# Kernel tuning notes

Hardware: AMD Instinct MI355X
Metric: run time of the kernel (lower is better)

The kernel has to match this reference:

```python
import jax, jax.numpy as jnp
import numpy as np

N = 100000      # nodes_num
E = 1600000     # edges (avg degree 16)
D_IN = 256
D_OUT = 128
EPS = 1e-3      # keras BatchNormalization default epsilon
LEAKY = 0.2     # tf.nn.leaky_relu default alpha


def setup_inputs() -> dict:
    key = jax.random.key(0)
    ks = jax.random.split(key, 6)
    x = jax.random.normal(ks[0], (N, D_IN), jnp.float32)
    w = jax.random.normal(ks[1], (D_IN, D_OUT), jnp.float32) / np.float32(np.sqrt(D_IN))
    w1 = jax.random.normal(ks[2], (D_IN, D_IN), jnp.float32) / np.float32(np.sqrt(D_IN))
    w2 = jax.random.normal(ks[3], (D_IN, D_IN), jnp.float32) / np.float32(np.sqrt(D_IN))
    rows = jnp.sort(jax.random.randint(ks[4], (E,), 0, N, jnp.int32))
    cols = jax.random.randint(ks[5], (E,), 0, N, jnp.int32)
    edge_vals = jnp.ones((E,), jnp.float32)
    return {"x": x, "w": w, "w1": w1, "w2": w2,
            "edge_vals": edge_vals, "rows": rows, "cols": cols}


def reference(x, w, w1, w2, edge_vals, rows, cols):
    # Batch norm (training mode: per-feature stats over node axis, gamma=1, beta=0)
    mean = jnp.mean(x, axis=0)
    var = jnp.var(x, axis=0)
    xn = (x - mean) * jax.lax.rsqrt(var + EPS)          # [N, D_IN]

    mapped = xn @ w                                      # [N, D_OUT]
    s1 = jnp.tanh(jnp.sum((xn @ w1) * xn, axis=1))       # [N] row score
    s2 = jnp.tanh(jnp.sum((xn @ w2) * xn, axis=1))       # [N] col score

    # sparse add of adj*s1[row] and adj*s2[col], then leaky_relu on edge values
    ev = edge_vals * (s1[rows] + s2[cols])               # [E]
    ev = jnp.where(ev > 0, ev, LEAKY * ev)

    # tf.sparse.softmax: softmax over the nonzero entries of each row
    m = jax.ops.segment_max(ev, rows, num_segments=N)    # [N]
    m = jnp.where(jnp.isfinite(m), m, 0.0)               # empty rows -> 0
    ex = jnp.exp(ev - m[rows])
    denom = jax.ops.segment_sum(ex, rows, num_segments=N)
    alpha = ex / denom[rows]                             # [E] edge softmax

    # SpMM: out[i] = sum_{e: rows[e]==i} alpha[e] * mapped[cols[e]]
    out = jax.ops.segment_sum(alpha[:, None] * mapped[cols], rows, num_segments=N)
    return out  # activation is identity (activation=None)
```

## Files before the change

kernel.cpp:

```cpp
#include <hip/hip_runtime.h>

#define D_IN 256
#define D_OUT 128
#define EPS_BN 1e-3f
#define LEAKY 0.2f

typedef unsigned short u16;
typedef unsigned int u32;
typedef u16 u16x4 __attribute__((ext_vector_type(4)));
typedef u16 u16x8 __attribute__((ext_vector_type(8)));
typedef __bf16 bf16x8 __attribute__((ext_vector_type(8)));
typedef float f32x4 __attribute__((ext_vector_type(4)));

__device__ __forceinline__ float bf2f(u16 u) {
    u32 v = ((u32)u) << 16;
    return __uint_as_float(v);
}
__device__ __forceinline__ u16 f2bf(float f) {
    u32 u = __float_as_uint(f);
    u32 r = (u + 0x7FFFu + ((u >> 16) & 1u)) >> 16;
    return (u16)r;
}

__device__ __forceinline__ void bar_lgkm() {
    asm volatile("s_waitcnt lgkmcnt(0)" ::: "memory");
    __builtin_amdgcn_s_barrier();
    asm volatile("" ::: "memory");
}

__global__ void colstats_k(const float* __restrict__ x, int n,
                           float* __restrict__ sums, float* __restrict__ sqs) {
    int c = threadIdx.x;
    float s = 0.f, q = 0.f;
    for (int r = blockIdx.x; r < n; r += gridDim.x) {
        float v = x[(size_t)r * D_IN + c];
        s += v;
        q += v * v;
    }
    atomicAdd(&sums[c], s);
    atomicAdd(&sqs[c], q);
}

__global__ void finalize_k(const float* __restrict__ sums, const float* __restrict__ sqs,
                           int n, float* __restrict__ mean, float* __restrict__ inv) {
    int c = threadIdx.x;
    float m = sums[c] / (float)n;
    float v = sqs[c] / (float)n - m * m;
    mean[c] = m;
    inv[c] = rsqrtf(v + EPS_BN);
}

__global__ void prep_w_k(const float* __restrict__ w1, const float* __restrict__ w2,
                         const float* __restrict__ w, u16* __restrict__ Bth,
                         u16* __restrict__ Btl, u16* __restrict__ Wth,
                         u16* __restrict__ Wtl) {
    int idx = blockIdx.x * 256 + threadIdx.x;
    int k = idx & 255;
    int nn = idx >> 8;
    if (nn < 512) {
        float v = (nn < 256) ? w1[(size_t)k * 256 + nn]
                             : w2[(size_t)k * 256 + (nn - 256)];
        u16 h = f2bf(v);
        u16 l = f2bf(v - bf2f(h));
        Bth[(size_t)nn * 256 + k] = h;
        Btl[(size_t)nn * 256 + k] = l;
    } else {
        int nm = nn - 512;
        float v = w[(size_t)k * D_OUT + nm];
        u16 h = f2bf(v);
        u16 l = f2bf(v - bf2f(h));
        Wth[(size_t)nm * 256 + k] = h;
        Wtl[(size_t)nm * 256 + k] = l;
    }
}

__device__ __forceinline__ int kmap(int v, int g, int j) {
    return (v == 0) ? (8 * g + j) : (16 * (j >> 2) + 4 * g + (j & 3));
}

__global__ void probe_k(int* __restrict__ flagp) {
    __shared__ float Ar[16][32];
    __shared__ float Br[32][16];
    __shared__ float Dr[16][16];
    int l = threadIdx.x;
    for (int i = l; i < 512; i += 64) {
        int r = i >> 5, k = i & 31;
        Ar[r][k] = (float)(((r * 5 + k * 3) % 11) - 5);
    }
    for (int i = l; i < 512; i += 64) {
        int k = i >> 4, c = i & 15;
        Br[k][c] = (float)(((k * 3 + c * 7) % 13) - 6);
    }
    __syncthreads();
    for (int i = l; i < 256; i += 64) {
        int r = i >> 4, c = i & 15;
        float s = 0.f;
        for (int k = 0; k < 32; ++k) s += Ar[r][k] * Br[k][c];
        Dr[r][c] = s;
    }
    __syncthreads();
    int g = l >> 4, c15 = l & 15;
    int found = -1;
    for (int combo = 0; combo < 4; ++combo) {
        int va = combo >> 1, vb = combo & 1;
        u16x8 af, bfv;
#pragma unroll
        for (int j = 0; j < 8; ++j) {
            af[j] = f2bf(Ar[c15][kmap(va, g, j)]);
            bfv[j] = f2bf(Br[kmap(vb, g, j)][c15]);
        }
        f32x4 d = {0.f, 0.f, 0.f, 0.f};
        d = __builtin_amdgcn_mfma_f32_16x16x32_bf16(
            __builtin_bit_cast(bf16x8, af), __builtin_bit_cast(bf16x8, bfv), d,
            0, 0, 0);
        bool ok = true;
#pragma unroll
        for (int r = 0; r < 4; ++r) ok = ok && (d[r] == Dr[g * 4 + r][c15]);
        if (found < 0 && __all(ok)) found = combo;
    }
    if (l == 0) flagp[0] = (found < 0) ? 0 : found;
}

__device__ __forceinline__ void stage_A(const float* __restrict__ x,
                                        const float* __restrict__ mean,
                                        const float* __restrict__ inv, int m0,
                                        int n, u16* Ah, u16* Al) {
    const int tid = threadIdx.x;
    for (int i = 0; i < 16; ++i) {
        int chunk = tid + (i << 8);
        int r = chunk >> 6;
        int c4 = (chunk & 63) << 2;
        int gr = m0 + r;
        bool ok = gr < n;
        float4 v = make_float4(0.f, 0.f, 0.f, 0.f);
        if (ok) v = *(const float4*)(x + (size_t)gr * D_IN + c4);
        float4 mn = *(const float4*)(mean + c4);
        float4 iv = *(const float4*)(inv + c4);
        float a0 = ok ? (v.x - mn.x) * iv.x : 0.f;
        float a1 = ok ? (v.y - mn.y) * iv.y : 0.f;
        float a2 = ok ? (v.z - mn.z) * iv.z : 0.f;
        float a3 = ok ? (v.w - mn.w) * iv.w : 0.f;
        u16 h0 = f2bf(a0), h1 = f2bf(a1), h2 = f2bf(a2), h3 = f2bf(a3);
        u16 l0 = f2bf(a0 - bf2f(h0)), l1 = f2bf(a1 - bf2f(h1));
        u16 l2 = f2bf(a2 - bf2f(h2)), l3 = f2bf(a3 - bf2f(h3));
        int off = (r << 9) + (((c4 << 1) ^ ((r & 7) << 4)));
        u16x4 hv = {h0, h1, h2, h3};
        u16x4 lv = {l0, l1, l2, l3};
        *(u16x4*)((char*)Ah + off) = hv;
        *(u16x4*)((char*)Al + off) = lv;
    }
}

__device__ __forceinline__ void ldb_regs(const u16* __restrict__ Gh,
                                         const u16* __restrict__ Gl, int n0,
                                         int k0, int tid, u16x8 (&hv)[2],
                                         u16x8 (&lv)[2]) {
#pragma unroll
    for (int i = 0; i < 2; ++i) {
        int chunk = tid + (i << 8);
        int nl = chunk >> 3;
        int k8 = (chunk & 7) << 3;
        size_t goff = (size_t)(n0 + nl) * 256 + k0 + k8;
        hv[i] = *(const u16x8*)(Gh + goff);
        lv[i] = *(const u16x8*)(Gl + goff);
    }
}
__device__ __forceinline__ void stb_lds(u16* Bh, u16* Bl, int tid,
                                        const u16x8 (&hv)[2],
                                        const u16x8 (&lv)[2]) {
#pragma unroll
    for (int i = 0; i < 2; ++i) {
        int chunk = tid + (i << 8);
        int nl = chunk >> 3;
        int k8 = (chunk & 7) << 3;
        int off = (nl << 7) + (((k8 << 1) ^ ((nl & 7) << 4)));
        *(u16x8*)((char*)Bh + off) = hv[i];
        *(u16x8*)((char*)Bl + off) = lv[i];
    }
}

template <int V>
__device__ __forceinline__ bf16x8 ld_frag(const u16* plane, int rowByteBase,
                                          int swz, int kbyte, int g) {
    const char* p = (const char*)plane + rowByteBase;
    if constexpr (V == 0) {
        u16x8 v = *(const u16x8*)(p + ((kbyte + (g << 4)) ^ swz));
        return __builtin_bit_cast(bf16x8, v);
    } else {
        u16x4 a = *(const u16x4*)(p + ((kbyte + (g << 3)) ^ swz));
        u16x4 b = *(const u16x4*)(p + ((kbyte + 32 + (g << 3)) ^ swz));
        u16x8 v;
        v[0] = a[0]; v[1] = a[1]; v[2] = a[2]; v[3] = a[3];
        v[4] = b[0]; v[5] = b[1]; v[6] = b[2]; v[7] = b[3];
        return __builtin_bit_cast(bf16x8, v);
    }
}

template <int VA, int VB>
__device__ __forceinline__ void comp_kt(const u16* Ah, const u16* Al,
                                        const u16* Bh, const u16* Bl, int kt,
                                        int wm, int wn, int c15, int g,
                                        f32x4 (&acc)[2][2]) {
#pragma unroll
    for (int kk = 0; kk < 2; ++kk) {
        int kbA = kt * 128 + kk * 64;
        int kbB = kk * 64;
        bf16x8 ah[2], alf[2], bhf[2], blf[2];
#pragma unroll
        for (int mf = 0; mf < 2; ++mf) {
            int row = wm * 32 + mf * 16 + c15;
            int swz = (row & 7) << 4;
            ah[mf] = ld_frag<VA>(Ah, row << 9, swz, kbA, g);
            alf[mf] = ld_frag<VA>(Al, row << 9, swz, kbA, g);
        }
#pragma unroll
        for (int nf = 0; nf < 2; ++nf) {
            int nl = wn * 32 + nf * 16 + c15;
            int swz = (nl & 7) << 4;
            bhf[nf] = ld_frag<VB>(Bh, nl << 7, swz, kbB, g);
            blf[nf] = ld_frag<VB>(Bl, nl << 7, swz, kbB, g);
        }
#pragma unroll
        for (int mf = 0; mf < 2; ++mf)
#pragma unroll
            for (int nf = 0; nf < 2; ++nf) {
                acc[mf][nf] = __builtin_amdgcn_mfma_f32_16x16x32_bf16(
                    ah[mf], bhf[nf], acc[mf][nf], 0, 0, 0);
                acc[mf][nf] = __builtin_amdgcn_mfma_f32_16x16x32_bf16(
                    ah[mf], blf[nf], acc[mf][nf], 0, 0, 0);
                acc[mf][nf] = __builtin_amdgcn_mfma_f32_16x16x32_bf16(
                    alf[mf], bhf[nf], acc[mf][nf], 0, 0, 0);
            }
    }
}

template <int VA, int VB>
__device__ __forceinline__ void quadmap_body(
    const float* __restrict__ x, const u16* __restrict__ Bth,
    const u16* __restrict__ Btl, const u16* __restrict__ Wth,
    const u16* __restrict__ Wtl, const float* __restrict__ mean,
    const float* __restrict__ inv, float* __restrict__ s1,
    float* __restrict__ s2, u16* __restrict__ mapped, int n, int mapCT,
    u16* Ah, u16* Al, u16* Bh, u16* Bl) {
    const int tid = threadIdx.x;
    const int lane = tid & 63, wave = tid >> 6;
    const int g = lane >> 4, c15 = lane & 15;
    const int wm = wave >> 1, wn = wave & 1;
    const int m0 = blockIdx.x * 64;

    stage_A(x, mean, inv, m0, n, Ah, Al);
    __syncthreads();

    u16x8 rbh[2], rbl[2];
    ldb_regs(Bth, Btl, 0, 0, tid, rbh, rbl);

    float sp[2][4] = {{0.f, 0.f, 0.f, 0.f}, {0.f, 0.f, 0.f, 0.f}};

    for (int jt = 0; jt < 8; ++jt) {
        f32x4 acc[2][2];
#pragma unroll
        for (int mf = 0; mf < 2; ++mf)
#pragma unroll
            for (int nf = 0; nf < 2; ++nf) acc[mf][nf] = (f32x4){0.f, 0.f, 0.f, 0.f};

        for (int kt = 0; kt < 4; ++kt) {
            bar_lgkm();
            stb_lds(Bh, Bl, tid, rbh, rbl);
            const u16 *sH, *sL;
            int nn0, nk0;
            if (kt < 3)      { sH = Bth; sL = Btl; nn0 = jt * 64;       nk0 = (kt + 1) * 64; }
            else if (jt < 7) { sH = Bth; sL = Btl; nn0 = (jt + 1) * 64; nk0 = 0; }
            else             { sH = Wth; sL = Wtl; nn0 = 0;             nk0 = 0; }
            ldb_regs(sH, sL, nn0, nk0, tid, rbh, rbl);
            bar_lgkm();
            comp_kt<VA, VB>(Ah, Al, Bh, Bl, kt, wm, wn, c15, g, acc);
        }

        int fcol0 = (jt & 3) << 6;
#pragma unroll
        for (int mf = 0; mf < 2; ++mf) {
#pragma unroll
            for (int nf = 0; nf < 2; ++nf) {
                int col = fcol0 + wn * 32 + nf * 16 + c15;
                float mn = mean[col], ivv = inv[col];
#pragma unroll
                for (int r = 0; r < 4; ++r) {
                    int grow = m0 + wm * 32 + mf * 16 + g * 4 + r;
                    float xv = 0.f;
                    if (grow < n) xv = (x[(size_t)grow * D_IN + col] - mn) * ivv;
                    sp[mf][r] = fmaf(acc[mf][nf][r], xv, sp[mf][r]);
                }
            }
        }
        if ((jt & 3) == 3) {
            float part[2][4];
#pragma unroll
            for (int mf = 0; mf < 2; ++mf)
#pragma unroll
                for (int r = 0; r < 4; ++r) {
                    float v = sp[mf][r];
                    v += __shfl_xor(v, 1);
                    v += __shfl_xor(v, 2);
                    v += __shfl_xor(v, 4);
                    v += __shfl_xor(v, 8);
                    part[mf][r] = v;
                    sp[mf][r] = 0.f;
                }
            float* scratch = (float*)Bh;
            bar_lgkm();
            if (c15 == 0) {
#pragma unroll
                for (int mf = 0; mf < 2; ++mf)
#pragma unroll
                    for (int r = 0; r < 4; ++r) {
                        int sidx = (((((wm << 2) | g) << 1) | mf) << 3) | (r << 1) | wn;
                        scratch[sidx] = part[mf][r];
                    }
            }
            bar_lgkm();
            if (wn == 0 && c15 == 0) {
                float* dst = (jt < 4) ? s1 : s2;
#pragma unroll
                for (int mf = 0; mf < 2; ++mf)
#pragma unroll
                    for (int r = 0; r < 4; ++r) {
                        int sidx = (((((wm << 2) | g) << 1) | mf) << 3) | (r << 1);
                        float tot = scratch[sidx] + scratch[sidx | 1];
                        int grow = m0 + wm * 32 + mf * 16 + g * 4 + r;
                        if (grow < n) dst[grow] = tanhf(tot);
                    }
            }
        }
    }

    const int tiles = mapCT >> 6;
    for (int t = 0; t < tiles; ++t) {
        f32x4 acc[2][2];
#pragma unroll
        for (int mf = 0; mf < 2; ++mf)
#pragma unroll
            for (int nf = 0; nf < 2; ++nf) acc[mf][nf] = (f32x4){0.f, 0.f, 0.f, 0.f};

        for (int kt = 0; kt < 4; ++kt) {
            bar_lgkm();
            stb_lds(Bh, Bl, tid, rbh, rbl);
            int nn0 = (kt < 3) ? t * 64 : ((t + 1 < tiles) ? (t + 1) * 64 : t * 64);
            int nk0 = (kt < 3) ? (kt + 1) * 64 : 0;
            ldb_regs(Wth, Wtl, nn0, nk0, tid, rbh, rbl);
            bar_lgkm();
            comp_kt<VA, VB>(Ah, Al, Bh, Bl, kt, wm, wn, c15, g, acc);
        }
#pragma unroll
        for (int mf = 0; mf < 2; ++mf)
#pragma unroll
            for (int nf = 0; nf < 2; ++nf) {
                int si = t * 64 + wn * 32 + nf * 16 + c15;
#pragma unroll
                for (int r = 0; r < 4; ++r) {
                    int grow = m0 + wm * 32 + mf * 16 + g * 4 + r;
                    if (grow < n)
                        mapped[(size_t)grow * mapCT + si] = f2bf(acc[mf][nf][r]);
                }
            }
    }
}

__global__ __launch_bounds__(256) void quadmap_mfma_k(
    const float* __restrict__ x, const u16* __restrict__ Bth,
    const u16* __restrict__ Btl, const u16* __restrict__ Wth,
    const u16* __restrict__ Wtl, const float* __restrict__ mean,
    const float* __restrict__ inv, float* __restrict__ s1,
    float* __restrict__ s2, u16* __restrict__ mapped,
    const int* __restrict__ flagp, int n, int mapCT) {
    __shared__ u16 Ah[64 * 256];
    __shared__ u16 Al[64 * 256];
    __shared__ u16 Bh[64 * 64];
    __shared__ u16 Bl[64 * 64];
    int v = flagp[0];
    if (v == 1)
        quadmap_body<0, 1>(x, Bth, Btl, Wth, Wtl, mean, inv, s1, s2, mapped, n, mapCT, Ah, Al, Bh, Bl);
    else if (v == 2)
        quadmap_body<1, 0>(x, Bth, Btl, Wth, Wtl, mean, inv, s1, s2, mapped, n, mapCT, Ah, Al, Bh, Bl);
    else if (v == 3)
        quadmap_body<1, 1>(x, Bth, Btl, Wth, Wtl, mean, inv, s1, s2, mapped, n, mapCT, Ah, Al, Bh, Bl);
    else
        quadmap_body<0, 0>(x, Bth, Btl, Wth, Wtl, mean, inv, s1, s2, mapped, n, mapCT, Ah, Al, Bh, Bl);
}

template <int VA, int VB>
__device__ __forceinline__ void map_body(
    const float* __restrict__ x, const u16* __restrict__ Wth,
    const u16* __restrict__ Wtl, const float* __restrict__ mean,
    const float* __restrict__ inv, u16* __restrict__ mapped, int n, int c0,
    int CT, u16* Ah, u16* Al, u16* Bh, u16* Bl) {
    const int tid = threadIdx.x;
    const int lane = tid & 63, wave = tid >> 6;
    const int g = lane >> 4, c15 = lane & 15;
    const int wm = wave >> 1, wn = wave & 1;
    const int m0 = blockIdx.x * 64;

    stage_A(x, mean, inv, m0, n, Ah, Al);
    __syncthreads();

    u16x8 rbh[2], rbl[2];
    ldb_regs(Wth, Wtl, c0, 0, tid, rbh, rbl);

    const int tiles = CT >> 6;
    for (int t = 0; t < tiles; ++t) {
        f32x4 acc[2][2];
#pragma unroll
        for (int mf = 0; mf < 2; ++mf)
#pragma unroll
            for (int nf = 0; nf < 2; ++nf) acc[mf][nf] = (f32x4){0.f, 0.f, 0.f, 0.f};

        for (int kt = 0; kt < 4; ++kt) {
            bar_lgkm();
            stb_lds(Bh, Bl, tid, rbh, rbl);
            int nn0 = (kt < 3) ? c0 + t * 64
                               : c0 + ((t + 1 < tiles) ? (t + 1) * 64 : t * 64);
            int nk0 = (kt < 3) ? (kt + 1) * 64 : 0;
            ldb_regs(Wth, Wtl, nn0, nk0, tid, rbh, rbl);
            bar_lgkm();
            comp_kt<VA, VB>(Ah, Al, Bh, Bl, kt, wm, wn, c15, g, acc);
        }
#pragma unroll
        for (int mf = 0; mf < 2; ++mf)
#pragma unroll
            for (int nf = 0; nf < 2; ++nf) {
                int si = t * 64 + wn * 32 + nf * 16 + c15;
#pragma unroll
                for (int r = 0; r < 4; ++r) {
                    int grow = m0 + wm * 32 + mf * 16 + g * 4 + r;
                    if (grow < n) mapped[(size_t)grow * CT + si] = f2bf(acc[mf][nf][r]);
                }
            }
    }
}

__global__ __launch_bounds__(256) void map_mfma_k(
    const float* __restrict__ x, const u16* __restrict__ Wth,
    const u16* __restrict__ Wtl, const float* __restrict__ mean,
    const float* __restrict__ inv, u16* __restrict__ mapped, int n, int c0,
    int CT, const int* __restrict__ flagp) {
    __shared__ u16 Ah[64 * 256];
    __shared__ u16 Al[64 * 256];
    __shared__ u16 Bh[64 * 64];
    __shared__ u16 Bl[64 * 64];
    int v = flagp[0];
    if (v == 1) map_body<0, 1>(x, Wth, Wtl, mean, inv, mapped, n, c0, CT, Ah, Al, Bh, Bl);
    else if (v == 2) map_body<1, 0>(x, Wth, Wtl, mean, inv, mapped, n, c0, CT, Ah, Al, Bh, Bl);
    else if (v == 3) map_body<1, 1>(x, Wth, Wtl, mean, inv, mapped, n, c0, CT, Ah, Al, Bh, Bl);
    else map_body<0, 0>(x, Wth, Wtl, mean, inv, mapped, n, c0, CT, Ah, Al, Bh, Bl);
}

template <typename OT>
__global__ __launch_bounds__(256) void gemm_map_k(const float* __restrict__ x,
                                                  const float* __restrict__ w,
                                                  const float* __restrict__ mean,
                                                  const float* __restrict__ inv,
                                                  OT* __restrict__ outp, int n,
                                                  int c0, int CT) {
    __shared__ float As[64][68];
    __shared__ float Bs[64][68];
    const int tid = threadIdx.x;
    const int tx = tid & 15, ty = tid >> 4;
    const int m0 = blockIdx.x * 64;
    const int tiles = (CT + 63) >> 6;

    for (int t = 0; t < tiles; ++t) {
        const int jt = c0 + (t << 6);
        float acc[4][4];
#pragma unroll
        for (int a = 0; a < 4; ++a)
#pragma unroll
            for (int b = 0; b < 4; ++b) acc[a][b] = 0.f;

        for (int kt = 0; kt < D_IN; kt += 64) {
#pragma unroll
            for (int i = 0; i < 4; ++i) {
                int f4 = tid + 256 * i;
                int r = f4 >> 4;
                int c4 = (f4 & 15) << 2;
                float4 o;
                int gr = m0 + r;
                if (gr < n) {
                    float4 v = *(const float4*)(x + (size_t)gr * D_IN + kt + c4);
                    float4 mn = *(const float4*)(mean + kt + c4);
                    float4 iv = *(const float4*)(inv + kt + c4);
                    o.x = (v.x - mn.x) * iv.x;
                    o.y = (v.y - mn.y) * iv.y;
                    o.z = (v.z - mn.z) * iv.z;
                    o.w = (v.w - mn.w) * iv.w;
                } else {
                    o = make_float4(0.f, 0.f, 0.f, 0.f);
                }
                *(float4*)&As[r][c4] = o;
            }
#pragma unroll
            for (int i = 0; i < 4; ++i) {
                int f4 = tid + 256 * i;
                int r = f4 >> 4;
                int c4 = (f4 & 15) << 2;
                int jc = jt + c4;
                float4 bv = (jc < D_OUT)
                                ? *(const float4*)(w + (size_t)(kt + r) * D_OUT + jc)
                                : make_float4(0.f, 0.f, 0.f, 0.f);
                *(float4*)&Bs[r][c4] = bv;
            }
            __syncthreads();
#pragma unroll 8
            for (int k = 0; k < 64; ++k) {
                float4 bv = *(const float4*)&Bs[k][tx << 2];
                float a0 = As[(ty << 2) + 0][k];
                float a1 = As[(ty << 2) + 1][k];
                float a2 = As[(ty << 2) + 2][k];
                float a3 = As[(ty << 2) + 3][k];
                acc[0][0] = fmaf(a0, bv.x, acc[0][0]);
                acc[0][1] = fmaf(a0, bv.y, acc[0][1]);
                acc[0][2] = fmaf(a0, bv.z, acc[0][2]);
                acc[0][3] = fmaf(a0, bv.w, acc[0][3]);
                acc[1][0] = fmaf(a1, bv.x, acc[1][0]);
                acc[1][1] = fmaf(a1, bv.y, acc[1][1]);
                acc[1][2] = fmaf(a1, bv.z, acc[1][2]);
                acc[1][3] = fmaf(a1, bv.w, acc[1][3]);
                acc[2][0] = fmaf(a2, bv.x, acc[2][0]);
                acc[2][1] = fmaf(a2, bv.y, acc[2][1]);
                acc[2][2] = fmaf(a2, bv.z, acc[2][2]);
                acc[2][3] = fmaf(a2, bv.w, acc[2][3]);
                acc[3][0] = fmaf(a3, bv.x, acc[3][0]);
                acc[3][1] = fmaf(a3, bv.y, acc[3][1]);
                acc[3][2] = fmaf(a3, bv.z, acc[3][2]);
                acc[3][3] = fmaf(a3, bv.w, acc[3][3]);
            }
            __syncthreads();
        }
        int si = (jt - c0) + (tx << 2);
        if (si < CT) {
#pragma unroll
            for (int a = 0; a < 4; ++a) {
                int gm = m0 + (ty << 2) + a;
                if (gm < n) {
                    ushort4 pk;
                    pk.x = f2bf(acc[a][0]);
                    pk.y = f2bf(acc[a][1]);
                    pk.z = f2bf(acc[a][2]);
                    pk.w = f2bf(acc[a][3]);
                    *(ushort4*)((u16*)outp + (size_t)gm * CT + si) = pk;
                }
            }
        }
    }
}

__global__ void build_rowptr_k(const int* __restrict__ rows, int E, int n,
                               int* __restrict__ rp) {
    int e = blockIdx.x * blockDim.x + threadIdx.x;
    if (e >= E) return;
    int r = rows[e];
    int prev = (e == 0) ? -1 : rows[e - 1];
    for (int q = prev + 1; q <= r; ++q) rp[q] = e;
    if (e == E - 1) {
        for (int q = r + 1; q <= n; ++q) rp[q] = E;
    }
}

template <bool WRITE_ALPHA>
__global__ __launch_bounds__(256) void row_softmax_k(
    const int* __restrict__ row_ptr, const int* __restrict__ cols,
    const float* __restrict__ ev, const float* __restrict__ s1,
    const float* __restrict__ s2, float* __restrict__ rmax,
    float* __restrict__ rsm, float* __restrict__ alpha, int n) {
    int wave = threadIdx.x >> 6;
    int lane = threadIdx.x & 63;
    int row = blockIdx.x * 4 + wave;
    if (row >= n) return;
    int e0 = row_ptr[row], e1 = row_ptr[row + 1];
    if (e0 >= e1) {
        if (lane == 0) {
            rmax[row] = 0.f;
            rsm[row] = 0.f;
        }
        return;
    }
    float s1r = s1[row];
    float mx = -1e30f;
    for (int e = e0 + lane; e < e1; e += 64) {
        float v = ev[e] * (s1r + s2[cols[e]]);
        v = v > 0.f ? v : LEAKY * v;
        mx = fmaxf(mx, v);
    }
#pragma unroll
    for (int off = 32; off; off >>= 1) mx = fmaxf(mx, __shfl_xor(mx, off));
    float sm = 0.f;
    for (int e = e0 + lane; e < e1; e += 64) {
        float v = ev[e] * (s1r + s2[cols[e]]);
        v = v > 0.f ? v : LEAKY * v;
        sm += __expf(v - mx);
    }
#pragma unroll
    for (int off = 32; off; off >>= 1) sm += __shfl_xor(sm, off);
    float rsm_v = 1.f / sm;
    if (lane == 0) {
        rmax[row] = mx;
        rsm[row] = rsm_v;
    }
    if constexpr (WRITE_ALPHA) {
        for (int e = e0 + lane; e < e1; e += 64) {
            float v = ev[e] * (s1r + s2[cols[e]]);
            v = v > 0.f ? v : LEAKY * v;
            alpha[e] = __expf(v - mx) * rsm_v;
        }
    }
}

template <bool HAS_ALPHA>
__global__ __launch_bounds__(256) void attn_gather2_k(
    const int* __restrict__ row_ptr, const int* __restrict__ cols,
    const float* __restrict__ alpha, const float* __restrict__ ev,
    const float* __restrict__ s1, const float* __restrict__ s2,
    const float* __restrict__ rmax, const float* __restrict__ rsm,
    const u16* __restrict__ mapped, float* __restrict__ outp, int n, int c0,
    int CT) {
    const int wave = threadIdx.x >> 6;
    const int lane = threadIdx.x & 63;
    const int row = blockIdx.x * 4 + wave;
    if (row >= n) return;
    const int e0 = row_ptr[row], e1 = row_ptr[row + 1];
    float* orow = outp + (size_t)row * D_OUT + c0;
    const int nu = CT >> 1;
    const bool act = lane < nu;
    if (e0 >= e1) {
        if (act) *(float2*)(orow + (lane << 1)) = make_float2(0.f, 0.f);
        return;
    }
    float s1r = 0.f, mxv = 0.f, rsv = 0.f;
    if constexpr (!HAS_ALPHA) {
        s1r = s1[row];
        mxv = rmax[row];
        rsv = rsm[row];
    }
    const u32* map32 = (const u32*)mapped;
    float ox = 0.f, oy = 0.f;
    int e = e0;
    while (e < e1) {
        int cnt = min(e1 - e, 64);
        int ce = 0;
        float ae = 0.f;
        if (lane < cnt) {
            int ee = e + lane;
            ce = cols[ee];
            if constexpr (HAS_ALPHA) {
                ae = alpha[ee];
            } else {
                float v = ev[ee] * (s1r + s2[ce]);
                v = v > 0.f ? v : LEAKY * v;
                ae = __expf(v - mxv) * rsv;
            }
        }
        for (int j0 = 0; j0 < cnt; j0 += 8) {
            int cv[8];
            float av[8];
            u32 mv[8];
#pragma unroll
            for (int j = 0; j < 8; ++j) {
                cv[j] = __shfl(ce, j0 + j);
                av[j] = __shfl(ae, j0 + j);
            }
#pragma unroll
            for (int j = 0; j < 8; ++j)
                mv[j] = act ? map32[(size_t)cv[j] * nu + lane] : 0u;
#pragma unroll
            for (int j = 0; j < 8; ++j) {
                ox = fmaf(av[j], bf2f((u16)(mv[j] & 0xffffu)), ox);
                oy = fmaf(av[j], bf2f((u16)(mv[j] >> 16)), oy);
            }
        }
        e += cnt;
    }
    if (act) *(float2*)(orow + (lane << 1)) = make_float2(ox, oy);
}

extern "C" void kernel_launch(void* const* d_in, const int* in_sizes, int n_in,
                              void* d_out, int out_size, void* d_ws, size_t ws_size,
                              hipStream_t stream) {
    const float* x  = (const float*)d_in[0];
    const float* w  = (const float*)d_in[1];
    const float* w1 = (const float*)d_in[2];
    const float* w2 = (const float*)d_in[3];
    const float* ev = (const float*)d_in[4];
    const int* rows = (const int*)d_in[5];
    const int* cols = (const int*)d_in[6];
    float* out = (float*)d_out;

    const int N = in_sizes[0] / D_IN;
    const int E = in_sizes[4];

    char* base = (char*)d_ws;
    size_t off = 0;
    auto alloc = [&](size_t bytes) -> char* {
        off = (off + 255) & ~(size_t)255;
        char* p = base + off;
        off += bytes;
        return p;
    };
    float* sums  = (float*)alloc(256 * 4);
    float* sqs   = (float*)alloc(256 * 4);
    float* mean  = (float*)alloc(256 * 4);
    float* inv   = (float*)alloc(256 * 4);
    float* s1    = (float*)alloc((size_t)N * 4);
    float* s2    = (float*)alloc((size_t)N * 4);
    float* rmax  = (float*)alloc((size_t)N * 4);
    float* rsm   = (float*)alloc((size_t)N * 4);
    int* row_ptr = (int*)alloc((size_t)(N + 1) * 4);
    int* flag    = (int*)alloc(256);
    u16* Bth = (u16*)alloc((size_t)512 * 256 * 2);
    u16* Btl = (u16*)alloc((size_t)512 * 256 * 2);
    u16* Wth = (u16*)alloc((size_t)128 * 256 * 2);
    u16* Wtl = (u16*)alloc((size_t)128 * 256 * 2);
    size_t head0 = off;

    size_t alpha_bytes = (size_t)E * 4;
    auto fits_alpha = [&](size_t mapped_bytes) {
        size_t o = (head0 + 255) & ~(size_t)255;
        o += alpha_bytes;
        o = (o + 255) & ~(size_t)255;
        return o + mapped_bytes <= ws_size;
    };
    auto fits_noalpha = [&](size_t mapped_bytes) {
        size_t o = (head0 + 255) & ~(size_t)255;
        return o + mapped_bytes <= ws_size;
    };

    bool has_alpha;
    int CT;
    if (fits_alpha((size_t)N * 128 * 2)) {
        has_alpha = true; CT = 128;
    } else if (fits_alpha((size_t)N * 64 * 2)) {
        has_alpha = true; CT = 64;
    } else if (fits_noalpha((size_t)N * 32 * 2)) {
        has_alpha = false; CT = 32;
    } else if (fits_noalpha((size_t)N * 16 * 2)) {
        has_alpha = false; CT = 16;
    } else {
        has_alpha = false; CT = 8;
    }
    float* alpha = has_alpha ? (float*)alloc(alpha_bytes) : nullptr;
    u16* mapped = (u16*)alloc((size_t)N * CT * 2);

    hipMemsetAsync(sums, 0, 512 * sizeof(float), stream);
    colstats_k<<<512, 256, 0, stream>>>(x, N, sums, sqs);
    finalize_k<<<1, 256, 0, stream>>>(sums, sqs, N, mean, inv);
    prep_w_k<<<640, 256, 0, stream>>>(w1, w2, w, Bth, Btl, Wth, Wtl);
    probe_k<<<1, 64, 0, stream>>>(flag);

    int qb = (N + 63) / 64;
    int mapCT = (CT >= 64) ? CT : 0;
    quadmap_mfma_k<<<qb, 256, 0, stream>>>(x, Bth, Btl, Wth, Wtl, mean, inv, s1,
                                           s2, mapped, flag, N, mapCT);

    build_rowptr_k<<<(E + 255) / 256, 256, 0, stream>>>(rows, E, N, row_ptr);
    int ab = (N + 3) / 4;
    if (has_alpha) {
        row_softmax_k<true><<<ab, 256, 0, stream>>>(row_ptr, cols, ev, s1, s2,
                                                    rmax, rsm, alpha, N);
    } else {
        row_softmax_k<false><<<ab, 256, 0, stream>>>(row_ptr, cols, ev, s1, s2,
                                                     rmax, rsm, nullptr, N);
    }

    if (CT == 128) {
        attn_gather2_k<true><<<ab, 256, 0, stream>>>(
            row_ptr, cols, alpha, ev, s1, s2, rmax, rsm, mapped, out, N, 0, CT);
    } else if (CT == 64) {
        attn_gather2_k<true><<<ab, 256, 0, stream>>>(
            row_ptr, cols, alpha, ev, s1, s2, rmax, rsm, mapped, out, N, 0, 64);
        map_mfma_k<<<qb, 256, 0, stream>>>(x, Wth, Wtl, mean, inv, mapped, N, 64,
                                           64, flag);
        attn_gather2_k<true><<<ab, 256, 0, stream>>>(
            row_ptr, cols, alpha, ev, s1, s2, rmax, rsm, mapped, out, N, 64, 64);
    } else {
        for (int c0 = 0; c0 < D_OUT; c0 += CT) {
            gemm_map_k<u16><<<qb, 256, 0, stream>>>(x, w, mean, inv, mapped, N,
                                                    c0, CT);
            attn_gather2_k<false><<<ab, 256, 0, stream>>>(
                row_ptr, cols, nullptr, ev, s1, s2, rmax, rsm, mapped, out, N,
                c0, CT);
        }
    }
}
```

Before: 584.7 us.

## Double-buffer B tiles in the quadmap MFMA kernel with 512 threads

The fused batch-norm plus bilinear-score plus mapping GEMM kernel now runs 8 waves per block, each wave owning a 32x16 output slice. B is streamed in half-size K=32 chunks through two ping-pong LDS buffers, so the global prefetch, the LDS store and the MFMA compute of consecutive chunks overlap with one barrier per step instead of two. The launch moves to 512 threads with launch bounds (512,4). Separately, the column-stats kernel reads float4 per thread across four row phases to cut load instructions. The trade-off is more barriers per K, a smaller per-wave tile (less register reuse of A fragments) and extra register pressure from the occupancy hint.

```diff
diff --git a/kernel.cpp b/kernel.cpp
--- a/kernel.cpp
+++ b/kernel.cpp
@@ -30,15 +30,25 @@
 
 __global__ void colstats_k(const float* __restrict__ x, int n,
                            float* __restrict__ sums, float* __restrict__ sqs) {
-    int c = threadIdx.x;
-    float s = 0.f, q = 0.f;
-    for (int r = blockIdx.x; r < n; r += gridDim.x) {
-        float v = x[(size_t)r * D_IN + c];
-        s += v;
-        q += v * v;
-    }
-    atomicAdd(&sums[c], s);
-    atomicAdd(&sqs[c], q);
+    int c4 = (threadIdx.x & 63) << 2;
+    int rp = threadIdx.x >> 6;
+    float s0 = 0.f, s1 = 0.f, s2 = 0.f, s3 = 0.f;
+    float q0 = 0.f, q1 = 0.f, q2 = 0.f, q3 = 0.f;
+    for (int r = blockIdx.x * 4 + rp; r < n; r += gridDim.x * 4) {
+        float4 v = *(const float4*)(x + (size_t)r * D_IN + c4);
+        s0 += v.x; q0 += v.x * v.x;
+        s1 += v.y; q1 += v.y * v.y;
+        s2 += v.z; q2 += v.z * v.z;
+        s3 += v.w; q3 += v.w * v.w;
+    }
+    atomicAdd(&sums[c4 + 0], s0);
+    atomicAdd(&sums[c4 + 1], s1);
+    atomicAdd(&sums[c4 + 2], s2);
+    atomicAdd(&sums[c4 + 3], s3);
+    atomicAdd(&sqs[c4 + 0], q0);
+    atomicAdd(&sqs[c4 + 1], q1);
+    atomicAdd(&sqs[c4 + 2], q2);
+    atomicAdd(&sqs[c4 + 3], q3);
 }
 
 __global__ void finalize_k(const float* __restrict__ sums, const float* __restrict__ sqs,
@@ -121,13 +131,15 @@
     if (l == 0) flagp[0] = (found < 0) ? 0 : found;
 }
 
+template <int NT>
 __device__ __forceinline__ void stage_A(const float* __restrict__ x,
                                         const float* __restrict__ mean,
                                         const float* __restrict__ inv, int m0,
                                         int n, u16* Ah, u16* Al) {
     const int tid = threadIdx.x;
-    for (int i = 0; i < 16; ++i) {
-        int chunk = tid + (i << 8);
+#pragma unroll
+    for (int i = 0; i < 4096 / NT; ++i) {
+        int chunk = tid + i * NT;
         int r = chunk >> 6;
         int c4 = (chunk & 63) << 2;
         int gr = m0 + r;
@@ -151,34 +163,6 @@
     }
 }
 
-__device__ __forceinline__ void ldb_regs(const u16* __restrict__ Gh,
-                                         const u16* __restrict__ Gl, int n0,
-                                         int k0, int tid, u16x8 (&hv)[2],
-                                         u16x8 (&lv)[2]) {
-#pragma unroll
-    for (int i = 0; i < 2; ++i) {
-        int chunk = tid + (i << 8);
-        int nl = chunk >> 3;
-        int k8 = (chunk & 7) << 3;
-        size_t goff = (size_t)(n0 + nl) * 256 + k0 + k8;
-        hv[i] = *(const u16x8*)(Gh + goff);
-        lv[i] = *(const u16x8*)(Gl + goff);
-    }
-}
-__device__ __forceinline__ void stb_lds(u16* Bh, u16* Bl, int tid,
-                                        const u16x8 (&hv)[2],
-                                        const u16x8 (&lv)[2]) {
-#pragma unroll
-    for (int i = 0; i < 2; ++i) {
-        int chunk = tid + (i << 8);
-        int nl = chunk >> 3;
-        int k8 = (chunk & 7) << 3;
-        int off = (nl << 7) + (((k8 << 1) ^ ((nl & 7) << 4)));
-        *(u16x8*)((char*)Bh + off) = hv[i];
-        *(u16x8*)((char*)Bl + off) = lv[i];
-    }
-}
-
 template <int V>
 __device__ __forceinline__ bf16x8 ld_frag(const u16* plane, int rowByteBase,
                                           int swz, int kbyte, int g) {
@@ -196,42 +180,99 @@
     }
 }
 
+__device__ __forceinline__ void ldb_half(const u16* __restrict__ Gh,
+                                         const u16* __restrict__ Gl, int n0,
+                                         int k0, int tid, u16x4& hv, u16x4& lv) {
+    int nl = tid >> 3;
+    int k4 = (tid & 7) << 2;
+    size_t goff = (size_t)(n0 + nl) * 256 + k0 + k4;
+    hv = *(const u16x4*)(Gh + goff);
+    lv = *(const u16x4*)(Gl + goff);
+}
+__device__ __forceinline__ void stb_half(u16* Bh, u16* Bl, int tid,
+                                         const u16x4& hv, const u16x4& lv) {
+    int nl = tid >> 3;
+    int kb = (tid & 7) << 3;
+    int off = (nl << 6) + (kb ^ (((nl >> 1) & 3) << 4));
+    *(u16x4*)((char*)Bh + off) = hv;
+    *(u16x4*)((char*)Bl + off) = lv;
+}
+template <int V>
+__device__ __forceinline__ bf16x8 ld_bfrag(const u16* Bp, int nl, int g) {
+    const char* p = (const char*)Bp + (nl << 6);
+    int swz = ((nl >> 1) & 3) << 4;
+    if constexpr (V == 0) {
+        u16x8 v = *(const u16x8*)(p + ((g << 4) ^ swz));
+        return __builtin_bit_cast(bf16x8, v);
+    } else {
+        u16x4 a = *(const u16x4*)(p + ((g << 3) ^ swz));
+        u16x4 b = *(const u16x4*)(p + ((32 + (g << 3)) ^ swz));
+        u16x8 v;
+        v[0] = a[0]; v[1] = a[1]; v[2] = a[2]; v[3] = a[3];
+        v[4] = b[0]; v[5] = b[1]; v[6] = b[2]; v[7] = b[3];
+        return __builtin_bit_cast(bf16x8, v);
+    }
+}
+
 template <int VA, int VB>
-__device__ __forceinline__ void comp_kt(const u16* Ah, const u16* Al,
-                                        const u16* Bh, const u16* Bl, int kt,
-                                        int wm, int wn, int c15, int g,
-                                        f32x4 (&acc)[2][2]) {
-#pragma unroll
-    for (int kk = 0; kk < 2; ++kk) {
-        int kbA = kt * 128 + kk * 64;
-        int kbB = kk * 64;
-        bf16x8 ah[2], alf[2], bhf[2], blf[2];
-#pragma unroll
-        for (int mf = 0; mf < 2; ++mf) {
-            int row = wm * 32 + mf * 16 + c15;
-            int swz = (row & 7) << 4;
-            ah[mf] = ld_frag<VA>(Ah, row << 9, swz, kbA, g);
-            alf[mf] = ld_frag<VA>(Al, row << 9, swz, kbA, g);
-        }
-#pragma unroll
-        for (int nf = 0; nf < 2; ++nf) {
-            int nl = wn * 32 + nf * 16 + c15;
-            int swz = (nl & 7) << 4;
-            bhf[nf] = ld_frag<VB>(Bh, nl << 7, swz, kbB, g);
-            blf[nf] = ld_frag<VB>(Bl, nl << 7, swz, kbB, g);
-        }
-#pragma unroll
-        for (int mf = 0; mf < 2; ++mf)
-#pragma unroll
-            for (int nf = 0; nf < 2; ++nf) {
-                acc[mf][nf] = __builtin_amdgcn_mfma_f32_16x16x32_bf16(
-                    ah[mf], bhf[nf], acc[mf][nf], 0, 0, 0);
-                acc[mf][nf] = __builtin_amdgcn_mfma_f32_16x16x32_bf16(
-                    ah[mf], blf[nf], acc[mf][nf], 0, 0, 0);
-                acc[mf][nf] = __builtin_amdgcn_mfma_f32_16x16x32_bf16(
-                    alf[mf], bhf[nf], acc[mf][nf], 0, 0, 0);
-            }
-    }
+__device__ __forceinline__ void comp_half(const u16* Ah, const u16* Al,
+                                          const u16* Bh, const u16* Bl, int kbA,
+                                          int wm, int wn, int c15, int g,
+                                          f32x4 (&acc)[2]) {
+    bf16x8 ah[2], alf[2];
+#pragma unroll
+    for (int mf = 0; mf < 2; ++mf) {
+        int row = wm * 32 + mf * 16 + c15;
+        int swz = (row & 7) << 4;
+        ah[mf] = ld_frag<VA>(Ah, row << 9, swz, kbA, g);
+        alf[mf] = ld_frag<VA>(Al, row << 9, swz, kbA, g);
+    }
+    int nl = wn * 16 + c15;
+    bf16x8 bh = ld_bfrag<VB>(Bh, nl, g);
+    bf16x8 bl = ld_bfrag<VB>(Bl, nl, g);
+#pragma unroll
+    for (int mf = 0; mf < 2; ++mf) {
+        acc[mf] = __builtin_amdgcn_mfma_f32_16x16x32_bf16(ah[mf], bh, acc[mf], 0, 0, 0);
+        acc[mf] = __builtin_amdgcn_mfma_f32_16x16x32_bf16(ah[mf], bl, acc[mf], 0, 0, 0);
+        acc[mf] = __builtin_amdgcn_mfma_f32_16x16x32_bf16(alf[mf], bh, acc[mf], 0, 0, 0);
+    }
+}
+
+__device__ __forceinline__ void nxt_src(int u, int mapCT,
+                                        const u16* __restrict__ Bth,
+                                        const u16* __restrict__ Btl,
+                                        const u16* __restrict__ Wth,
+                                        const u16* __restrict__ Wtl,
+                                        const u16*& Gh, const u16*& Gl, int& n0,
+                                        int& k0) {
+    if (u < 64) {
+        Gh = Bth; Gl = Btl;
+        n0 = (u >> 3) << 6;
+        k0 = (u & 7) << 5;
+    } else {
+        int um = u - 64;
+        int t = um >> 3;
+        int tmax = (mapCT >= 64) ? ((mapCT >> 6) - 1) : 0;
+        if (t > tmax) t = tmax;
+        Gh = Wth; Gl = Wtl;
+        n0 = t << 6;
+        k0 = (um & 7) << 5;
+    }
+}
+
+template <int VA, int VB>
+__device__ __forceinline__ void pipe_step(const u16* Ah, const u16* Al,
+                                          const u16* Bch, const u16* Bcl,
+                                          u16* Bwh, u16* Bwl, u16x4& h, u16x4& l,
+                                          const u16* __restrict__ Gh,
+                                          const u16* __restrict__ Gl, int n0,
+                                          int k0, int kbA, int tid, int wm,
+                                          int wn, int c15, int g,
+                                          f32x4 (&acc)[2]) {
+    stb_half(Bwh, Bwl, tid, h, l);
+    ldb_half(Gh, Gl, n0, k0, tid, h, l);
+    comp_half<VA, VB>(Ah, Al, Bch, Bcl, kbA, wm, wn, c15, g, acc);
+    bar_lgkm();
 }
 
 template <int VA, int VB>
@@ -241,54 +282,60 @@
     const u16* __restrict__ Wtl, const float* __restrict__ mean,
     const float* __restrict__ inv, float* __restrict__ s1,
     float* __restrict__ s2, u16* __restrict__ mapped, int n, int mapCT,
-    u16* Ah, u16* Al, u16* Bh, u16* Bl) {
+    u16* Ah, u16* Al, u16* Bh0, u16* Bl0, u16* Bh1, u16* Bl1) {
     const int tid = threadIdx.x;
     const int lane = tid & 63, wave = tid >> 6;
     const int g = lane >> 4, c15 = lane & 15;
-    const int wm = wave >> 1, wn = wave & 1;
+    const int wm = wave >> 2, wn = wave & 3;
     const int m0 = blockIdx.x * 64;
 
-    stage_A(x, mean, inv, m0, n, Ah, Al);
+    stage_A<512>(x, mean, inv, m0, n, Ah, Al);
     __syncthreads();
 
-    u16x8 rbh[2], rbl[2];
-    ldb_regs(Bth, Btl, 0, 0, tid, rbh, rbl);
+    u16x4 hA, lA, hB, lB;
+    {
+        const u16 *Gh, *Gl; int n0, k0;
+        nxt_src(0, mapCT, Bth, Btl, Wth, Wtl, Gh, Gl, n0, k0);
+        ldb_half(Gh, Gl, n0, k0, tid, hA, lA);
+        nxt_src(1, mapCT, Bth, Btl, Wth, Wtl, Gh, Gl, n0, k0);
+        ldb_half(Gh, Gl, n0, k0, tid, hB, lB);
+        stb_half(Bh0, Bl0, tid, hA, lA);
+        nxt_src(2, mapCT, Bth, Btl, Wth, Wtl, Gh, Gl, n0, k0);
+        ldb_half(Gh, Gl, n0, k0, tid, hA, lA);
+        bar_lgkm();
+    }
 
     float sp[2][4] = {{0.f, 0.f, 0.f, 0.f}, {0.f, 0.f, 0.f, 0.f}};
+    float* red = (float*)Bh1;
 
     for (int jt = 0; jt < 8; ++jt) {
-        f32x4 acc[2][2];
-#pragma unroll
-        for (int mf = 0; mf < 2; ++mf)
-#pragma unroll
-            for (int nf = 0; nf < 2; ++nf) acc[mf][nf] = (f32x4){0.f, 0.f, 0.f, 0.f};
-
-        for (int kt = 0; kt < 4; ++kt) {
-            bar_lgkm();
-            stb_lds(Bh, Bl, tid, rbh, rbl);
-            const u16 *sH, *sL;
-            int nn0, nk0;
-            if (kt < 3)      { sH = Bth; sL = Btl; nn0 = jt * 64;       nk0 = (kt + 1) * 64; }
-            else if (jt < 7) { sH = Bth; sL = Btl; nn0 = (jt + 1) * 64; nk0 = 0; }
-            else             { sH = Wth; sL = Wtl; nn0 = 0;             nk0 = 0; }
-            ldb_regs(sH, sL, nn0, nk0, tid, rbh, rbl);
-            bar_lgkm();
-            comp_kt<VA, VB>(Ah, Al, Bh, Bl, kt, wm, wn, c15, g, acc);
-        }
-
-        int fcol0 = (jt & 3) << 6;
-#pragma unroll
-        for (int mf = 0; mf < 2; ++mf) {
-#pragma unroll
-            for (int nf = 0; nf < 2; ++nf) {
-                int col = fcol0 + wn * 32 + nf * 16 + c15;
-                float mn = mean[col], ivv = inv[col];
+        const int u0 = jt * 8;
+        f32x4 acc[2];
+        acc[0] = (f32x4){0.f, 0.f, 0.f, 0.f};
+        acc[1] = (f32x4){0.f, 0.f, 0.f, 0.f};
+
+#pragma unroll
+        for (int sp2 = 0; sp2 < 4; ++sp2) {
+            const u16 *Gh, *Gl; int n0, k0;
+            nxt_src(u0 + sp2 * 2 + 3, mapCT, Bth, Btl, Wth, Wtl, Gh, Gl, n0, k0);
+            pipe_step<VA, VB>(Ah, Al, Bh0, Bl0, Bh1, Bl1, hB, lB, Gh, Gl, n0, k0,
+                              (sp2 * 2) * 64, tid, wm, wn, c15, g, acc);
+            nxt_src(u0 + sp2 * 2 + 4, mapCT, Bth, Btl, Wth, Wtl, Gh, Gl, n0, k0);
+            pipe_step<VA, VB>(Ah, Al, Bh1, Bl1, Bh0, Bl0, hA, lA, Gh, Gl, n0, k0,
+                              (sp2 * 2 + 1) * 64, tid, wm, wn, c15, g, acc);
+        }
+
+        {
+            int col = ((jt & 3) << 6) + wn * 16 + c15;
+            float mn = mean[col], ivv = inv[col];
+#pragma unroll
+            for (int mf = 0; mf < 2; ++mf) {
 #pragma unroll
                 for (int r = 0; r < 4; ++r) {
                     int grow = m0 + wm * 32 + mf * 16 + g * 4 + r;
                     float xv = 0.f;
                     if (grow < n) xv = (x[(size_t)grow * D_IN + col] - mn) * ivv;
-                    sp[mf][r] = fmaf(acc[mf][nf][r], xv, sp[mf][r]);
+                    sp[mf][r] = fmaf(acc[mf][r], xv, sp[mf][r]);
                 }
             }
         }
@@ -306,15 +353,14 @@
                     part[mf][r] = v;
                     sp[mf][r] = 0.f;
                 }
-            float* scratch = (float*)Bh;
-            bar_lgkm();
             if (c15 == 0) {
 #pragma unroll
                 for (int mf = 0; mf < 2; ++mf)
 #pragma unroll
                     for (int r = 0; r < 4; ++r) {
-                        int sidx = (((((wm << 2) | g) << 1) | mf) << 3) | (r << 1) | wn;
-                        scratch[sidx] = part[mf][r];
+                        int sidx = ((((((wm << 2) | g) << 1) | mf) << 4)) |
+                                   (r << 2) | wn;
+                        red[sidx] = part[mf][r];
                     }
             }
             bar_lgkm();
@@ -324,48 +370,49 @@
                 for (int mf = 0; mf < 2; ++mf)
 #pragma unroll
                     for (int r = 0; r < 4; ++r) {
-                        int sidx = (((((wm << 2) | g) << 1) | mf) << 3) | (r << 1);
-                        float tot = scratch[sidx] + scratch[sidx | 1];
+                        int sidx = ((((((wm << 2) | g) << 1) | mf) << 4)) |
+                                   (r << 2);
+                        float tot = (red[sidx] + red[sidx | 1]) +
+                                    (red[sidx | 2] + red[sidx | 3]);
                         int grow = m0 + wm * 32 + mf * 16 + g * 4 + r;
                         if (grow < n) dst[grow] = tanhf(tot);
                     }
             }
+            bar_lgkm();
         }
     }
 
     const int tiles = mapCT >> 6;
     for (int t = 0; t < tiles; ++t) {
-        f32x4 acc[2][2];
-#pragma unroll
-        for (int mf = 0; mf < 2; ++mf)
-#pragma unroll
-            for (int nf = 0; nf < 2; ++nf) acc[mf][nf] = (f32x4){0.f, 0.f, 0.f, 0.f};
-
-        for (int kt = 0; kt < 4; ++kt) {
-            bar_lgkm();
-            stb_lds(Bh, Bl, tid, rbh, rbl);
-            int nn0 = (kt < 3) ? t * 64 : ((t + 1 < tiles) ? (t + 1) * 64 : t * 64);
-            int nk0 = (kt < 3) ? (kt + 1) * 64 : 0;
-            ldb_regs(Wth, Wtl, nn0, nk0, tid, rbh, rbl);
-            bar_lgkm();
-            comp_kt<VA, VB>(Ah, Al, Bh, Bl, kt, wm, wn, c15, g, acc);
-        }
-#pragma unroll
-        for (int mf = 0; mf < 2; ++mf)
-#pragma unroll
-            for (int nf = 0; nf < 2; ++nf) {
-                int si = t * 64 + wn * 32 + nf * 16 + c15;
-#pragma unroll
-                for (int r = 0; r < 4; ++r) {
-                    int grow = m0 + wm * 32 + mf * 16 + g * 4 + r;
-                    if (grow < n)
-                        mapped[(size_t)grow * mapCT + si] = f2bf(acc[mf][nf][r]);
-                }
-            }
-    }
-}
-
-__global__ __launch_bounds__(256) void quadmap_mfma_k(
+        const int u0 = 64 + t * 8;
+        f32x4 acc[2];
+        acc[0] = (f32x4){0.f, 0.f, 0.f, 0.f};
+        acc[1] = (f32x4){0.f, 0.f, 0.f, 0.f};
+
+#pragma unroll
+        for (int sp2 = 0; sp2 < 4; ++sp2) {
+            const u16 *Gh, *Gl; int n0, k0;
+            nxt_src(u0 + sp2 * 2 + 3, mapCT, Bth, Btl, Wth, Wtl, Gh, Gl, n0, k0);
+            pipe_step<VA, VB>(Ah, Al, Bh0, Bl0, Bh1, Bl1, hB, lB, Gh, Gl, n0, k0,
+                              (sp2 * 2) * 64, tid, wm, wn, c15, g, acc);
+            nxt_src(u0 + sp2 * 2 + 4, mapCT, Bth, Btl, Wth, Wtl, Gh, Gl, n0, k0);
+            pipe_step<VA, VB>(Ah, Al, Bh1, Bl1, Bh0, Bl0, hA, lA, Gh, Gl, n0, k0,
+                              (sp2 * 2 + 1) * 64, tid, wm, wn, c15, g, acc);
+        }
+        int si = t * 64 + wn * 16 + c15;
+#pragma unroll
+        for (int mf = 0; mf < 2; ++mf) {
+#pragma unroll
+            for (int r = 0; r < 4; ++r) {
+                int grow = m0 + wm * 32 + mf * 16 + g * 4 + r;
+                if (grow < n)
+                    mapped[(size_t)grow * mapCT + si] = f2bf(acc[mf][r]);
+            }
+        }
+    }
+}
+
+__global__ __launch_bounds__(512, 4) void quadmap_mfma_k(
     const float* __restrict__ x, const u16* __restrict__ Bth,
     const u16* __restrict__ Btl, const u16* __restrict__ Wth,
     const u16* __restrict__ Wtl, const float* __restrict__ mean,
@@ -374,17 +421,84 @@
     const int* __restrict__ flagp, int n, int mapCT) {
     __shared__ u16 Ah[64 * 256];
     __shared__ u16 Al[64 * 256];
-    __shared__ u16 Bh[64 * 64];
-    __shared__ u16 Bl[64 * 64];
+    __shared__ u16 Bh0[64 * 32];
+    __shared__ u16 Bl0[64 * 32];
+    __shared__ u16 Bh1[64 * 32];
+    __shared__ u16 Bl1[64 * 32];
     int v = flagp[0];
     if (v == 1)
-        quadmap_body<0, 1>(x, Bth, Btl, Wth, Wtl, mean, inv, s1, s2, mapped, n, mapCT, Ah, Al, Bh, Bl);
+        quadmap_body<0, 1>(x, Bth, Btl, Wth, Wtl, mean, inv, s1, s2, mapped, n, mapCT, Ah, Al, Bh0, Bl0, Bh1, Bl1);
     else if (v == 2)
-        quadmap_body<1, 0>(x, Bth, Btl, Wth, Wtl, mean, inv, s1, s2, mapped, n, mapCT, Ah, Al, Bh, Bl);
+        quadmap_body<1, 0>(x, Bth, Btl, Wth, Wtl, mean, inv, s1, s2, mapped, n, mapCT, Ah, Al, Bh0, Bl0, Bh1, Bl1);
     else if (v == 3)
-        quadmap_body<1, 1>(x, Bth, Btl, Wth, Wtl, mean, inv, s1, s2, mapped, n, mapCT, Ah, Al, Bh, Bl);
+        quadmap_body<1, 1>(x, Bth, Btl, Wth, Wtl, mean, inv, s1, s2, mapped, n, mapCT, Ah, Al, Bh0, Bl0, Bh1, Bl1);
     else
-        quadmap_body<0, 0>(x, Bth, Btl, Wth, Wtl, mean, inv, s1, s2, mapped, n, mapCT, Ah, Al, Bh, Bl);
+        quadmap_body<0, 0>(x, Bth, Btl, Wth, Wtl, mean, inv, s1, s2, mapped, n, mapCT, Ah, Al, Bh0, Bl0, Bh1, Bl1);
+}
+
+__device__ __forceinline__ void ldb_regs(const u16* __restrict__ Gh,
+                                         const u16* __restrict__ Gl, int n0,
+                                         int k0, int tid, u16x8 (&hv)[2],
+                                         u16x8 (&lv)[2]) {
+#pragma unroll
+    for (int i = 0; i < 2; ++i) {
+        int chunk = tid + (i << 8);
+        int nl = chunk >> 3;
+        int k8 = (chunk & 7) << 3;
+        size_t goff = (size_t)(n0 + nl) * 256 + k0 + k8;
+        hv[i] = *(const u16x8*)(Gh + goff);
+        lv[i] = *(const u16x8*)(Gl + goff);
+    }
+}
+__device__ __forceinline__ void stb_lds(u16* Bh, u16* Bl, int tid,
+                                        const u16x8 (&hv)[2],
+                                        const u16x8 (&lv)[2]) {
+#pragma unroll
+    for (int i = 0; i < 2; ++i) {
+        int chunk = tid + (i << 8);
+        int nl = chunk >> 3;
+        int k8 = (chunk & 7) << 3;
+        int off = (nl << 7) + (((k8 << 1) ^ ((nl & 7) << 4)));
+        *(u16x8*)((char*)Bh + off) = hv[i];
+        *(u16x8*)((char*)Bl + off) = lv[i];
+    }
+}
+template <int VA, int VB>
+__device__ __forceinline__ void comp_kt(const u16* Ah, const u16* Al,
+                                        const u16* Bh, const u16* Bl, int kt,
+                                        int wm, int wn, int c15, int g,
+                                        f32x4 (&acc)[2][2]) {
+#pragma unroll
+    for (int kk = 0; kk < 2; ++kk) {
+        int kbA = kt * 128 + kk * 64;
+        int kbB = kk * 64;
+        bf16x8 ah[2], alf[2], bhf[2], blf[2];
+#pragma unroll
+        for (int mf = 0; mf < 2; ++mf) {
+            int row = wm * 32 + mf * 16 + c15;
+            int swz = (row & 7) << 4;
+            ah[mf] = ld_frag<VA>(Ah, row << 9, swz, kbA, g);
+            alf[mf] = ld_frag<VA>(Al, row << 9, swz, kbA, g);
+        }
+#pragma unroll
+        for (int nf = 0; nf < 2; ++nf) {
+            int nl = wn * 32 + nf * 16 + c15;
+            int swz = (nl & 7) << 4;
+            bhf[nf] = ld_frag<VB>(Bh, nl << 7, swz, kbB, g);
+            blf[nf] = ld_frag<VB>(Bl, nl << 7, swz, kbB, g);
+        }
+#pragma unroll
+        for (int mf = 0; mf < 2; ++mf)
+#pragma unroll
+            for (int nf = 0; nf < 2; ++nf) {
+                acc[mf][nf] = __builtin_amdgcn_mfma_f32_16x16x32_bf16(
+                    ah[mf], bhf[nf], acc[mf][nf], 0, 0, 0);
+                acc[mf][nf] = __builtin_amdgcn_mfma_f32_16x16x32_bf16(
+                    ah[mf], blf[nf], acc[mf][nf], 0, 0, 0);
+                acc[mf][nf] = __builtin_amdgcn_mfma_f32_16x16x32_bf16(
+                    alf[mf], bhf[nf], acc[mf][nf], 0, 0, 0);
+            }
+    }
 }
 
 template <int VA, int VB>
@@ -399,7 +513,7 @@
     const int wm = wave >> 1, wn = wave & 1;
     const int m0 = blockIdx.x * 64;
 
-    stage_A(x, mean, inv, m0, n, Ah, Al);
+    stage_A<256>(x, mean, inv, m0, n, Ah, Al);
     __syncthreads();
 
     u16x8 rbh[2], rbl[2];
@@ -755,7 +869,7 @@
 
     int qb = (N + 63) / 64;
     int mapCT = (CT >= 64) ? CT : 0;
-    quadmap_mfma_k<<<qb, 256, 0, stream>>>(x, Bth, Btl, Wth, Wtl, mean, inv, s1,
+    quadmap_mfma_k<<<qb, 512, 0, stream>>>(x, Bth, Btl, Wth, Wtl, mean, inv, s1,
                                            s2, mapped, flag, N, mapCT);
 
     build_rowptr_k<<<(E + 255) / 256, 256, 0, stream>>>(rows, E, N, row_ptr);
```

Result: slower. 720.1 us (+23.2%).
